# Kernel optimization log

Hardware: AMD Instinct MI355X
Metric: run time of the kernel (lower is better)

Reference implementation:

```python
import jax, jax.numpy as jnp
import numpy as np

B = 512      # batch (len(missing_type))
HALF = 12    # prompt_length // 3
D = 12       # prompt_depth
DT = 512     # text embed dim
DI = 768     # image embed dim
E = DT + DI  # 1280, concat dim
R = 16
H = E // R    # 80
HC = DT // R  # 32
EPS = 1e-5


def _ln(x, g, b):
    m = jnp.mean(x, -1, keepdims=True)
    v = jnp.mean((x - m) ** 2, -1, keepdims=True)
    return (x - m) * jax.lax.rsqrt(v + EPS) * g + b


def _mlp(x, w1, b1, w2, b2):
    return jax.nn.gelu(x @ w1 + b1, approximate=False) @ w2 + b2


def setup_inputs() -> dict:
    key = jax.random.key(0)
    ks = jax.random.split(key, 20)
    n = lambda k, s: jax.random.normal(k, s, dtype=jnp.float32) * 0.02
    return {
        "missing_type": jax.random.randint(ks[0], (B,), 0, 3),
        "vpc": n(ks[1], (HALF, DI)), "vpm": n(ks[2], (HALF, DI)),
        "tpc": n(ks[3], (HALF, DT)), "tpm": n(ks[4], (HALF, DT)),
        "cpc": n(ks[5], (HALF, DT)), "cpi": n(ks[6], (HALF, DT)), "cpt": n(ks[7], (HALF, DT)),
        "ln_img_g": jnp.ones((D, E)), "ln_img_b": jnp.zeros((D, E)),
        "ln_txt_g": jnp.ones((D, E)), "ln_txt_b": jnp.zeros((D, E)),
        "img_w1": n(ks[8], (D, E, H)), "img_b1": jnp.zeros((D, H)),
        "img_w2": n(ks[9], (D, H, DI)), "img_b2": jnp.zeros((D, DI)),
        "txt_w1": n(ks[10], (D, E, H)), "txt_b1": jnp.zeros((D, H)),
        "txt_w2": n(ks[11], (D, H, DT)), "txt_b2": jnp.zeros((D, DT)),
        "cimg_w1": n(ks[12], (DT, HC)), "cimg_b1": jnp.zeros((HC,)),
        "cimg_w2": n(ks[13], (HC, DI)), "cimg_b2": jnp.zeros((DI,)),
        "ctxt_w1": n(ks[14], (DT, HC)), "ctxt_b1": jnp.zeros((HC,)),
        "ctxt_w2": n(ks[15], (HC, DT)), "ctxt_b2": jnp.zeros((DT,)),
    }


def reference(missing_type, vpc, vpm, tpc, tpm, cpc, cpi, cpt,
              ln_img_g, ln_img_b, ln_txt_g, ln_txt_b,
              img_w1, img_b1, img_w2, img_b2,
              txt_w1, txt_b1, txt_w2, txt_b2,
              cimg_w1, cimg_b1, cimg_w2, cimg_b2,
              ctxt_w1, ctxt_b1, ctxt_w2, ctxt_b2):
    depth = img_w1.shape[0]
    mt = missing_type
    # per-sample branch selection, vectorized over the batch
    img = jnp.where((mt == 2)[:, None, None], vpm[None], vpc[None])  # [B,HALF,768]
    txt = jnp.where((mt == 1)[:, None, None], tpm[None], tpc[None])  # [B,HALF,512]
    common = jnp.stack([cpc, cpi, cpt])[mt]                          # [B,HALF,512]
    imgs, txts = [], []
    for d in range(depth):  # sequential depth dependency
        x = jnp.concatenate([img, txt], -1)  # [B,HALF,1280]
        img = _mlp(_ln(x, ln_img_g[d], ln_img_b[d]), img_w1[d], img_b1[d], img_w2[d], img_b2[d])
        txt = _mlp(_ln(x, ln_txt_g[d], ln_txt_b[d]), txt_w1[d], txt_b1[d], txt_w2[d], txt_b2[d])
        imgs.append(img)
        txts.append(txt)
    # depth-0 prompts get the projected common prompt appended along tokens
    img0 = jnp.concatenate([imgs[0], _mlp(common, cimg_w1, cimg_b1, cimg_w2, cimg_b2)], axis=1)
    txt0 = jnp.concatenate([txts[0], _mlp(common, ctxt_w1, ctxt_b1, ctxt_w2, ctxt_b2)], axis=1)
    return (img0, txt0, jnp.stack(imgs[1:]), jnp.stack(txts[1:]))
```

## Files before the change

kernel.cpp:

```cpp
#include <hip/hip_runtime.h>

typedef unsigned int u32;
typedef unsigned short u16;

#define TPB 640
#define NSLOT_TOT 180
#define SLOT_F32 10240
#define CHAIN_DYN 92928

namespace {
constexpr size_t F_BLOB = 0;
constexpr size_t F_S1   = 1843200;
constexpr size_t F_T1   = 1845120;
constexpr size_t F_XI   = 1847040;
constexpr size_t F_XT   = 2178816;
constexpr size_t F_CI   = 2400000;
constexpr size_t F_CT   = 2427648;
constexpr size_t F_END  = 2446080;
constexpr size_t F_XI_U = 0, F_XT_U = 331776, F_CI_U = 552960, F_CT_U = 580608;
}

__device__ __forceinline__ float bflo(u32 u) { return __uint_as_float(u << 16); }
__device__ __forceinline__ float bfhi(u32 u) { return __uint_as_float(u & 0xffff0000u); }
__device__ __forceinline__ float gelu_f(float x) { return 0.5f * x * (1.0f + erff(x * 0.70710678118654752f)); }
__device__ __forceinline__ u16 f2bf(float f) {
    u32 u = __float_as_uint(f);
    u += 0x7fffu + ((u >> 16) & 1u);
    return (u16)(u >> 16);
}

struct P {
    const float *vpc, *vpm, *tpc, *tpm, *cpc, *cpi, *cpt;
    const float *lig, *lib, *ltg, *ltb;
    const float *iw1, *ib1, *iw2, *ib2;
    const float *tw1, *tb1, *tw2, *tb2;
    const float *ciw1, *cib1, *ciw2, *cib2;
    const float *ctw1, *ctb1, *ctw2, *ctb2;
    const u16 *blob;
    const float *s1, *t1;
    float *xi, *xt, *cimg, *ctxt;
};

__global__ __launch_bounds__(256) void prep_pack_kernel(P p, u32* blob32) {
    constexpr u32 N1 = 12u * 1280 * 80;
    constexpr u32 N2 = 12u * 80 * 640;
    u32 i = blockIdx.x * 256 + threadIdx.x;
    if (i < N1) {
        u32 j2 = i % 80, rem = i / 80;
        u32 k = rem % 1280, d = rem / 1280;
        u32 j0 = 2 * j2;
        const int path = (j0 >= 80);
        const float* W = (path ? p.tw1 : p.iw1) + ((size_t)(d * 1280) + k) * 80 + (j0 - 80 * path);
        float g = (path ? p.ltg : p.lig)[d * 1280 + k];
        float2 v = *reinterpret_cast<const float2*>(W);
        blob32[(size_t)d * 153600 + (size_t)k * 80 + j2] =
            (u32)f2bf(g * v.x) | ((u32)f2bf(g * v.y) << 16);
    } else {
        u32 ii = i - N1;
        if (ii >= N2) return;
        u32 c2 = ii % 640, rem = ii / 640;
        u32 k = rem % 80, d = rem / 80;
        u32 c0 = 2 * c2;
        const float* s = (c0 < 768) ? (p.iw2 + ((size_t)(d * 80) + k) * 768 + c0)
                                    : (p.tw2 + ((size_t)(d * 80) + k) * 512 + (c0 - 768));
        float2 v = *reinterpret_cast<const float2*>(s);
        blob32[(size_t)d * 153600 + 102400 + (size_t)k * 640 + c2] =
            (u32)f2bf(v.x) | ((u32)f2bf(v.y) << 16);
    }
}

__global__ __launch_bounds__(TPB) void prep_fold_kernel(P p, float* s1o, float* t1o) {
    __shared__ float sA[8][80], sB[8][80];
    const int tid = threadIdx.x;
    const int d = blockIdx.x >> 1, path = blockIdx.x & 1;
    const float* W1 = (path ? p.tw1 : p.iw1) + (size_t)d * 1280 * 80;
    const float* G  = (path ? p.ltg : p.lig) + d * 1280;
    const float* Bb = (path ? p.ltb : p.lib) + d * 1280;
    const int j = tid % 80, kc = tid / 80;
    float S = 0.f, T = 0.f;
    for (int k = kc * 160; k < kc * 160 + 160; ++k) {
        float w = W1[(size_t)k * 80 + j];
        S += G[k] * w; T += Bb[k] * w;
    }
    sA[kc][j] = S; sB[kc][j] = T;
    __syncthreads();
    if (tid < 80) {
        float Ss = 0.f, Ts = 0.f;
        #pragma unroll
        for (int q = 0; q < 8; ++q) { Ss += sA[q][tid]; Ts += sB[q][tid]; }
        s1o[d * 160 + path * 80 + tid] = Ss;
        t1o[d * 160 + path * 80 + tid] = Ts + (path ? p.tb1 : p.ib1)[d * 80 + tid];
    }
}

__device__ __forceinline__ void stage_slot(const u16* blob, float* buf, int sigma) {
    const int d = sigma / 15, s = sigma % 15;
    const char* gbase = (const char*)(blob + (size_t)d * 307200
                                      + (s < 10 ? (size_t)s * 20480 : 204800 + (size_t)(s - 10) * 20480));
    char* lbase = (char*)buf;
    const int lane = threadIdx.x & 63, wave = threadIdx.x >> 6;
    #pragma unroll
    for (int r = 0; r < 4; ++r) {
        const int q = r * 10 + wave;
        __builtin_amdgcn_global_load_lds(
            (const __attribute__((address_space(1))) void*)(gbase + q * 1024 + lane * 16),
            (__attribute__((address_space(3))) void*)(lbase + q * 1024), 16, 0, 0);
    }
}

#define SLOT_SYNC do { asm volatile("s_waitcnt vmcnt(0)" ::: "memory"); \
                       __builtin_amdgcn_sched_barrier(0); __syncthreads(); } while (0)

__global__ __launch_bounds__(TPB) void chain4_kernel(P p) {
    extern __shared__ float smem[];
    float* buf0 = smem;
    float* buf1 = smem + 10240;
    float* sx   = smem + 20480;
    float* part = smem + 21760;
    float* hh   = smem + 23040;
    float* redA = smem + 23200;
    float* redB = smem + 23210;
    float* st   = smem + 23220;

    const int tid = threadIdx.x, blk = blockIdx.x;

    if (blk < 36) {
        const int v = blk / 12, t = blk % 12;
        stage_slot(p.blob, buf0, 0);
        const float* is = (v == 2) ? p.vpm : p.vpc;
        const float* ts = (v == 1) ? p.tpm : p.tpc;
        for (int k = tid; k < 768; k += TPB) sx[k] = is[t * 768 + k];
        if (tid < 512) sx[768 + tid] = ts[t * 512 + tid];
        SLOT_SYNC;
        int cur = 0;
        const int jp = tid % 80, kc = tid / 80;

        for (int d = 0; d < 12; ++d) {
            {
                float x0 = sx[tid], x1 = sx[tid + 640];
                float s = x0 + x1, s2 = x0 * x0 + x1 * x1;
                #pragma unroll
                for (int off = 32; off > 0; off >>= 1) { s += __shfl_down(s, off); s2 += __shfl_down(s2, off); }
                if ((tid & 63) == 0) { redA[tid >> 6] = s; redB[tid >> 6] = s2; }
            }
            __syncthreads();
            if (tid == 0) {
                float S = 0.f, S2 = 0.f;
                #pragma unroll
                for (int w = 0; w < 10; ++w) { S += redA[w]; S2 += redB[w]; }
                float m = S * (1.0f / 1280.0f);
                float var = S2 * (1.0f / 1280.0f) - m * m;
                st[0] = m; st[1] = rsqrtf(var + 1e-5f);
            }
            float a0 = 0.f, a1 = 0.f, b0 = 0.f, b1 = 0.f;
            for (int s = 0; s < 10; ++s) {
                const int sig = d * 15 + s;
                if (sig + 1 < NSLOT_TOT) stage_slot(p.blob, cur ? buf0 : buf1, sig + 1);
                const u32* wp = (const u32*)(cur ? buf1 : buf0) + kc * 1280 + jp;
                const float* xs = sx + s * 128 + kc * 16;
                #pragma unroll
                for (int i = 0; i < 16; ++i) {
                    u32 w = wp[i * 80];
                    float xv = xs[i];
                    a0 += xv * bflo(w); a1 += xv * bfhi(w);
                }
                if (s == 9) { part[kc * 160 + 2 * jp] = a0; part[kc * 160 + 2 * jp + 1] = a1; }
                SLOT_SYNC; cur ^= 1;
            }
            if (tid < 160) {
                float y = 0.f;
                #pragma unroll
                for (int q = 0; q < 8; ++q) y += part[q * 160 + tid];
                const float m = st[0], rs = st[1];
                hh[tid] = gelu_f(rs * y - m * rs * p.s1[d * 160 + tid] + p.t1[d * 160 + tid]);
            }
            __syncthreads();
            for (int s = 10; s < 15; ++s) {
                const int sig = d * 15 + s;
                if (sig + 1 < NSLOT_TOT) stage_slot(p.blob, cur ? buf0 : buf1, sig + 1);
                const u32* wq = (const u32*)(cur ? buf1 : buf0) + tid;
                const float* hb = hh + ((tid >= 384) ? 80 : 0) + (s - 10) * 16;
                #pragma unroll
                for (int i = 0; i < 16; ++i) {
                    u32 w = wq[i * 640];
                    float hv = hb[i];
                    b0 += hv * bflo(w); b1 += hv * bfhi(w);
                }
                SLOT_SYNC; cur ^= 1;
            }
            {
                const int c0 = 2 * tid;
                const int pth = (c0 >= 768);
                const int cc = c0 - 768 * pth;
                const int Np = pth ? 512 : 768;
                const float* bb = (pth ? p.tb2 : p.ib2) + d * Np + cc;
                float o0 = b0 + bb[0], o1 = b1 + bb[1];
                sx[c0] = o0; sx[c0 + 1] = o1;
                float* xo = pth ? (p.xt + ((size_t)(d * 36) + blk) * 512 + cc)
                                : (p.xi + ((size_t)(d * 36) + blk) * 768 + cc);
                *reinterpret_cast<float2*>(xo) = make_float2(o0, o1);
            }
            __syncthreads();
        }
    } else {
        float* cx  = smem;
        float* ph  = smem + 512;
        float* hhl = smem + 768;
        const int rr = blk - 36, v = rr / 12, t = rr % 12;
        const float* cs = (v == 0) ? p.cpc : (v == 1) ? p.cpi : p.cpt;
        if (tid < 512) cx[tid] = cs[t * 512 + tid];
        __syncthreads();
        if (tid < 256) {
            const int o = tid & 63, kcq = tid >> 6;
            const int path = o >> 5, j = o & 31;
            const float* w = (path ? p.ctw1 : p.ciw1) + (size_t)(kcq * 128) * 32 + j;
            float a = 0.f;
            #pragma unroll 8
            for (int i = 0; i < 128; ++i) { a += cx[kcq * 128 + i] * (*w); w += 32; }
            ph[kcq * 64 + o] = a;
        }
        __syncthreads();
        if (tid < 64) {
            const int path = tid >> 5, j = tid & 31;
            float a = (path ? p.ctb1 : p.cib1)[j];
            #pragma unroll
            for (int q = 0; q < 4; ++q) a += ph[q * 64 + tid];
            hhl[tid] = gelu_f(a);
        }
        __syncthreads();
        for (int o = tid; o < 1280; o += TPB) {
            if (o < 768) {
                float a = p.cib2[o];
                #pragma unroll
                for (int k = 0; k < 32; ++k) a += hhl[k] * p.ciw2[k * 768 + o];
                p.cimg[rr * 768 + o] = a;
            } else {
                const int oo = o - 768;
                float a = p.ctb2[oo];
                #pragma unroll
                for (int k = 0; k < 32; ++k) a += hhl[32 + k] * p.ctw2[k * 512 + oo];
                p.ctxt[rr * 512 + oo] = a;
            }
        }
    }
}

__global__ __launch_bounds__(TPB) void chain_fb_kernel(P p) {
    __shared__ float smem[6592];
    float* sx   = smem;
    float* xln0 = smem + 1280;
    float* xln1 = smem + 2560;
    float* part = smem + 3840;
    float* hh   = smem + 6400;
    float* redA = smem + 6560;
    float* redB = smem + 6570;
    float* st   = smem + 6580;
    const int tid = threadIdx.x, blk = blockIdx.x;
    if (blk < 36) {
        const int v = blk / 12, t = blk % 12;
        const float* is = (v == 2) ? p.vpm : p.vpc;
        const float* ts = (v == 1) ? p.tpm : p.tpc;
        if (tid < 512) sx[768 + tid] = ts[t * 512 + tid];
        for (int k = tid; k < 768; k += TPB) sx[k] = is[t * 768 + k];
        __syncthreads();
        for (int d = 0; d < 12; ++d) {
            {
                float x0 = sx[tid], x1 = sx[tid + 640];
                float s = x0 + x1, s2 = x0 * x0 + x1 * x1;
                #pragma unroll
                for (int off = 32; off > 0; off >>= 1) { s += __shfl_down(s, off); s2 += __shfl_down(s2, off); }
                if ((tid & 63) == 0) { redA[tid >> 6] = s; redB[tid >> 6] = s2; }
            }
            __syncthreads();
            if (tid == 0) {
                float S = 0.f, S2 = 0.f;
                #pragma unroll
                for (int w = 0; w < 10; ++w) { S += redA[w]; S2 += redB[w]; }
                float m = S * (1.0f / 1280.0f);
                float var = S2 * (1.0f / 1280.0f) - m * m;
                st[0] = m; st[1] = rsqrtf(var + 1e-5f);
            }
            __syncthreads();
            const float m = st[0], rs = st[1];
            #pragma unroll
            for (int q = 0; q < 2; ++q) {
                const int k = tid + 640 * q;
                float xc = (sx[k] - m) * rs;
                xln0[k] = xc * p.lig[d * 1280 + k] + p.lib[d * 1280 + k];
                xln1[k] = xc * p.ltg[d * 1280 + k] + p.ltb[d * 1280 + k];
            }
            __syncthreads();
            {
                const int g = tid % 40, kcq = tid / 40;
                const int j0 = 4 * g;
                const float* xl = (j0 >= 80) ? xln1 : xln0;
                const int k0 = kcq * 80;
                float a0 = 0.f, a1 = 0.f, a2 = 0.f, a3 = 0.f;
                const float* wp = (j0 < 80) ? (p.iw1 + ((size_t)(d * 1280) + k0) * 80 + j0)
                                            : (p.tw1 + ((size_t)(d * 1280) + k0) * 80 + (j0 - 80));
                #pragma unroll 8
                for (int i = 0; i < 80; ++i) {
                    float4 w = *reinterpret_cast<const float4*>(wp);
                    float xv = xl[k0 + i];
                    a0 += xv * w.x; a1 += xv * w.y; a2 += xv * w.z; a3 += xv * w.w;
                    wp += 80;
                }
                *reinterpret_cast<float4*>(part + kcq * 160 + j0) = make_float4(a0, a1, a2, a3);
            }
            __syncthreads();
            if (tid < 160) {
                const int path = tid >= 80, j = tid - 80 * path;
                float a = (path ? p.tb1 : p.ib1)[d * 80 + j];
                #pragma unroll
                for (int q = 0; q < 16; ++q) a += part[q * 160 + tid];
                hh[tid] = gelu_f(a);
            }
            __syncthreads();
            {
                const int c = tid;
                const int pth = (c >= 384);
                const int cc = 2 * c - 768 * pth;
                const float* hb = hh + 80 * pth;
                const int Np = pth ? 512 : 768;
                const float* b2 = (pth ? p.tb2 : p.ib2) + d * Np + cc;
                float a0 = b2[0], a1 = b2[1];
                const float* wp = (pth ? p.tw2 + (size_t)(d * 80) * 512 : p.iw2 + (size_t)(d * 80) * 768) + cc;
                #pragma unroll 16
                for (int k = 0; k < 80; ++k) {
                    float2 w = *reinterpret_cast<const float2*>(wp);
                    float hv = hb[k];
                    a0 += hv * w.x; a1 += hv * w.y;
                    wp += Np;
                }
                sx[2 * c] = a0; sx[2 * c + 1] = a1;
                float* xo = pth ? (p.xt + ((size_t)(d * 36) + blk) * 512 + cc)
                                : (p.xi + ((size_t)(d * 36) + blk) * 768 + cc);
                *reinterpret_cast<float2*>(xo) = make_float2(a0, a1);
            }
            __syncthreads();
        }
    } else {
        float* cx  = smem;
        float* ph  = smem + 512;
        float* hhl = smem + 768;
        const int rr = blk - 36, v = rr / 12, t = rr % 12;
        const float* cs = (v == 0) ? p.cpc : (v == 1) ? p.cpi : p.cpt;
        if (tid < 512) cx[tid] = cs[t * 512 + tid];
        __syncthreads();
        if (tid < 256) {
            const int o = tid & 63, kcq = tid >> 6;
            const int path = o >> 5, j = o & 31;
            const float* w = (path ? p.ctw1 : p.ciw1) + (size_t)(kcq * 128) * 32 + j;
            float a = 0.f;
            #pragma unroll 8
            for (int i = 0; i < 128; ++i) { a += cx[kcq * 128 + i] * (*w); w += 32; }
            ph[kcq * 64 + o] = a;
        }
        __syncthreads();
        if (tid < 64) {
            const int path = tid >> 5, j = tid & 31;
            float a = (path ? p.ctb1 : p.cib1)[j];
            #pragma unroll
            for (int q = 0; q < 4; ++q) a += ph[q * 64 + tid];
            hhl[tid] = gelu_f(a);
        }
        __syncthreads();
        for (int o = tid; o < 1280; o += TPB) {
            if (o < 768) {
                float a = p.cib2[o];
                #pragma unroll
                for (int k = 0; k < 32; ++k) a += hhl[k] * p.ciw2[k * 768 + o];
                p.cimg[rr * 768 + o] = a;
            } else {
                const int oo = o - 768;
                float a = p.ctb2[oo];
                #pragma unroll
                for (int k = 0; k < 32; ++k) a += hhl[32 + k] * p.ctw2[k * 512 + oo];
                p.ctxt[rr * 512 + oo] = a;
            }
        }
    }
}

__global__ __launch_bounds__(256) void emit_kernel(const int* __restrict__ mt,
                                                   const float* __restrict__ xi,
                                                   const float* __restrict__ xt,
                                                   const float* __restrict__ cimg,
                                                   const float* __restrict__ ctxt,
                                                   float* __restrict__ out) {
    constexpr unsigned int C0 = 512u * 24 * 192;
    constexpr unsigned int C1 = 512u * 24 * 128;
    constexpr unsigned int C2 = 11u * 512 * 12 * 192;
    constexpr unsigned int C3 = 11u * 512 * 12 * 128;
    constexpr unsigned int TOT = C0 + C1 + C2 + C3;
    const unsigned int stride = gridDim.x * blockDim.x;
    for (unsigned int c = blockIdx.x * blockDim.x + threadIdx.x; c < TOT; c += stride) {
        const float* src;
        if (c < C0) {
            unsigned int b = c / 4608u, r = c % 4608u;
            unsigned int tok = r / 192u, col = (r % 192u) * 4u;
            int v = mt[b];
            src = (tok < 12u) ? xi + ((size_t)v * 12 + tok) * 768 + col
                              : cimg + ((size_t)v * 12 + (tok - 12u)) * 768 + col;
        } else if (c < C0 + C1) {
            unsigned int cc = c - C0;
            unsigned int b = cc / 3072u, r = cc % 3072u;
            unsigned int tok = r / 128u, col = (r % 128u) * 4u;
            int v = mt[b];
            src = (tok < 12u) ? xt + ((size_t)v * 12 + tok) * 512 + col
                              : ctxt + ((size_t)v * 12 + (tok - 12u)) * 512 + col;
        } else if (c < C0 + C1 + C2) {
            unsigned int cc = c - C0 - C1;
            unsigned int d = cc / 1179648u, r = cc % 1179648u;
            unsigned int b = r / 2304u, rr = r % 2304u;
            unsigned int tok = rr / 192u, col = (rr % 192u) * 4u;
            int v = mt[b];
            src = xi + ((size_t)(d + 1) * 36 + v * 12 + tok) * 768 + col;
        } else {
            unsigned int cc = c - C0 - C1 - C2;
            unsigned int d = cc / 786432u, r = cc % 786432u;
            unsigned int b = r / 1536u, rr = r % 1536u;
            unsigned int tok = rr / 128u, col = (rr % 128u) * 4u;
            int v = mt[b];
            src = xt + ((size_t)(d + 1) * 36 + v * 12 + tok) * 512 + col;
        }
        *reinterpret_cast<float4*>(out + (size_t)c * 4) = *reinterpret_cast<const float4*>(src);
    }
}

extern "C" void kernel_launch(void* const* d_in, const int* in_sizes, int n_in,
                              void* d_out, int out_size, void* d_ws, size_t ws_size,
                              hipStream_t stream) {
    const int* mt = (const int*)d_in[0];
    float* ws = (float*)d_ws;
    P p;
    p.vpc  = (const float*)d_in[1];
    p.vpm  = (const float*)d_in[2];
    p.tpc  = (const float*)d_in[3];
    p.tpm  = (const float*)d_in[4];
    p.cpc  = (const float*)d_in[5];
    p.cpi  = (const float*)d_in[6];
    p.cpt  = (const float*)d_in[7];
    p.lig  = (const float*)d_in[8];
    p.lib  = (const float*)d_in[9];
    p.ltg  = (const float*)d_in[10];
    p.ltb  = (const float*)d_in[11];
    p.iw1  = (const float*)d_in[12];
    p.ib1  = (const float*)d_in[13];
    p.iw2  = (const float*)d_in[14];
    p.ib2  = (const float*)d_in[15];
    p.tw1  = (const float*)d_in[16];
    p.tb1  = (const float*)d_in[17];
    p.tw2  = (const float*)d_in[18];
    p.tb2  = (const float*)d_in[19];
    p.ciw1 = (const float*)d_in[20];
    p.cib1 = (const float*)d_in[21];
    p.ciw2 = (const float*)d_in[22];
    p.cib2 = (const float*)d_in[23];
    p.ctw1 = (const float*)d_in[24];
    p.ctb1 = (const float*)d_in[25];
    p.ctw2 = (const float*)d_in[26];
    p.ctb2 = (const float*)d_in[27];

    const bool packed = (ws_size >= F_END * sizeof(float));
    if (packed) {
        p.blob = (const u16*)(ws + F_BLOB);
        p.s1   = ws + F_S1;
        p.t1   = ws + F_T1;
        p.xi   = ws + F_XI;
        p.xt   = ws + F_XT;
        p.cimg = ws + F_CI;
        p.ctxt = ws + F_CT;
        constexpr u32 NPAIR = 12u * 1280 * 80 + 12u * 80 * 640;
        prep_pack_kernel<<<dim3((NPAIR + 255) / 256), dim3(256), 0, stream>>>(p, (u32*)(ws + F_BLOB));
        prep_fold_kernel<<<dim3(24), dim3(TPB), 0, stream>>>(p, ws + F_S1, ws + F_T1);
        hipFuncSetAttribute((const void*)chain4_kernel,
                            hipFuncAttributeMaxDynamicSharedMemorySize, CHAIN_DYN);
        chain4_kernel<<<dim3(72), dim3(TPB), CHAIN_DYN, stream>>>(p);
    } else {
        p.blob = nullptr; p.s1 = nullptr; p.t1 = nullptr;
        p.xi   = ws + F_XI_U;
        p.xt   = ws + F_XT_U;
        p.cimg = ws + F_CI_U;
        p.ctxt = ws + F_CT_U;
        chain_fb_kernel<<<dim3(72), dim3(TPB), 0, stream>>>(p);
    }
    emit_kernel<<<dim3(4096), dim3(256), 0, stream>>>(mt, p.xi, p.xt, p.cimg, p.ctxt, (float*)d_out);
}
```

Before: 252.4 us.

## Switch weight staging to a triple-buffered ring with partial vmcnt waits

Replaces the double-buffered weight slot staging with a three-slot LDS ring that prefetches two slots ahead. Each slot now waits only with vmcnt(4), which lets the next slot's loads stay in flight across the barrier instead of draining all global loads. The per-depth hidden reduction and GELU step is folded into the first second-layer slot, so its separate full barrier goes away. In exchange the kernel uses more LDS per block and relies on fragile manual waitcnt and barrier ordering to stay correct.

```diff
diff --git a/kernel.cpp b/kernel.cpp
--- a/kernel.cpp
+++ b/kernel.cpp
@@ -6,7 +6,7 @@
 #define TPB 640
 #define NSLOT_TOT 180
 #define SLOT_F32 10240
-#define CHAIN_DYN 92928
+#define CHAIN_DYN 133888
 
 namespace {
 constexpr size_t F_BLOB = 0;
@@ -108,31 +108,37 @@
     }
 }
 
-#define SLOT_SYNC do { asm volatile("s_waitcnt vmcnt(0)" ::: "memory"); \
-                       __builtin_amdgcn_sched_barrier(0); __syncthreads(); } while (0)
-
-__global__ __launch_bounds__(TPB) void chain4_kernel(P p) {
+#define CWAIT4 do { asm volatile("s_waitcnt vmcnt(4) lgkmcnt(0)" ::: "memory"); \
+                    __builtin_amdgcn_sched_barrier(0); __builtin_amdgcn_s_barrier(); \
+                    __builtin_amdgcn_sched_barrier(0); } while (0)
+#define CWAIT0 do { asm volatile("s_waitcnt vmcnt(0) lgkmcnt(0)" ::: "memory"); \
+                    __builtin_amdgcn_sched_barrier(0); __builtin_amdgcn_s_barrier(); \
+                    __builtin_amdgcn_sched_barrier(0); } while (0)
+#define LBAR   do { asm volatile("s_waitcnt lgkmcnt(0)" ::: "memory"); \
+                    __builtin_amdgcn_sched_barrier(0); __builtin_amdgcn_s_barrier(); \
+                    __builtin_amdgcn_sched_barrier(0); } while (0)
+
+__global__ __launch_bounds__(TPB) void chain5_kernel(P p) {
     extern __shared__ float smem[];
-    float* buf0 = smem;
-    float* buf1 = smem + 10240;
-    float* sx   = smem + 20480;
-    float* part = smem + 21760;
-    float* hh   = smem + 23040;
-    float* redA = smem + 23200;
-    float* redB = smem + 23210;
-    float* st   = smem + 23220;
+    float* ring = smem;
+    float* sx   = smem + 30720;
+    float* part = smem + 32000;
+    float* hh   = smem + 33280;
+    float* redA = smem + 33440;
+    float* redB = smem + 33450;
+    float* st   = smem + 33460;
 
     const int tid = threadIdx.x, blk = blockIdx.x;
 
     if (blk < 36) {
         const int v = blk / 12, t = blk % 12;
-        stage_slot(p.blob, buf0, 0);
+        stage_slot(p.blob, ring, 0);
+        stage_slot(p.blob, ring + SLOT_F32, 1);
         const float* is = (v == 2) ? p.vpm : p.vpc;
         const float* ts = (v == 1) ? p.tpm : p.tpc;
         for (int k = tid; k < 768; k += TPB) sx[k] = is[t * 768 + k];
         if (tid < 512) sx[768 + tid] = ts[t * 512 + tid];
-        SLOT_SYNC;
-        int cur = 0;
+        CWAIT0;
         const int jp = tid % 80, kc = tid / 80;
 
         for (int d = 0; d < 12; ++d) {
@@ -143,7 +149,7 @@
                 for (int off = 32; off > 0; off >>= 1) { s += __shfl_down(s, off); s2 += __shfl_down(s2, off); }
                 if ((tid & 63) == 0) { redA[tid >> 6] = s; redB[tid >> 6] = s2; }
             }
-            __syncthreads();
+            LBAR;
             if (tid == 0) {
                 float S = 0.f, S2 = 0.f;
                 #pragma unroll
@@ -155,8 +161,9 @@
             float a0 = 0.f, a1 = 0.f, b0 = 0.f, b1 = 0.f;
             for (int s = 0; s < 10; ++s) {
                 const int sig = d * 15 + s;
-                if (sig + 1 < NSLOT_TOT) stage_slot(p.blob, cur ? buf0 : buf1, sig + 1);
-                const u32* wp = (const u32*)(cur ? buf1 : buf0) + kc * 1280 + jp;
+                if (sig == NSLOT_TOT - 1) { CWAIT0; } else { CWAIT4; }
+                if (sig + 2 < NSLOT_TOT) stage_slot(p.blob, ring + (size_t)((sig + 2) % 3) * SLOT_F32, sig + 2);
+                const u32* wp = (const u32*)(ring + (size_t)(sig % 3) * SLOT_F32) + kc * 1280 + jp;
                 const float* xs = sx + s * 128 + kc * 16;
                 #pragma unroll
                 for (int i = 0; i < 16; ++i) {
@@ -165,20 +172,22 @@
                     a0 += xv * bflo(w); a1 += xv * bfhi(w);
                 }
                 if (s == 9) { part[kc * 160 + 2 * jp] = a0; part[kc * 160 + 2 * jp + 1] = a1; }
-                SLOT_SYNC; cur ^= 1;
-            }
-            if (tid < 160) {
-                float y = 0.f;
-                #pragma unroll
-                for (int q = 0; q < 8; ++q) y += part[q * 160 + tid];
-                const float m = st[0], rs = st[1];
-                hh[tid] = gelu_f(rs * y - m * rs * p.s1[d * 160 + tid] + p.t1[d * 160 + tid]);
-            }
-            __syncthreads();
+            }
             for (int s = 10; s < 15; ++s) {
                 const int sig = d * 15 + s;
-                if (sig + 1 < NSLOT_TOT) stage_slot(p.blob, cur ? buf0 : buf1, sig + 1);
-                const u32* wq = (const u32*)(cur ? buf1 : buf0) + tid;
+                if (sig == NSLOT_TOT - 1) { CWAIT0; } else { CWAIT4; }
+                if (sig + 2 < NSLOT_TOT) stage_slot(p.blob, ring + (size_t)((sig + 2) % 3) * SLOT_F32, sig + 2);
+                if (s == 10) {
+                    if (tid < 160) {
+                        float y = 0.f;
+                        #pragma unroll
+                        for (int q = 0; q < 8; ++q) y += part[q * 160 + tid];
+                        const float m = st[0], rs = st[1];
+                        hh[tid] = gelu_f(rs * y - m * rs * p.s1[d * 160 + tid] + p.t1[d * 160 + tid]);
+                    }
+                    LBAR;
+                }
+                const u32* wq = (const u32*)(ring + (size_t)(sig % 3) * SLOT_F32) + tid;
                 const float* hb = hh + ((tid >= 384) ? 80 : 0) + (s - 10) * 16;
                 #pragma unroll
                 for (int i = 0; i < 16; ++i) {
@@ -186,7 +195,6 @@
                     float hv = hb[i];
                     b0 += hv * bflo(w); b1 += hv * bfhi(w);
                 }
-                SLOT_SYNC; cur ^= 1;
             }
             {
                 const int c0 = 2 * tid;
@@ -200,7 +208,7 @@
                                 : (p.xi + ((size_t)(d * 36) + blk) * 768 + cc);
                 *reinterpret_cast<float2*>(xo) = make_float2(o0, o1);
             }
-            __syncthreads();
+            LBAR;
         }
     } else {
         float* cx  = smem;
@@ -474,9 +482,9 @@
         constexpr u32 NPAIR = 12u * 1280 * 80 + 12u * 80 * 640;
         prep_pack_kernel<<<dim3((NPAIR + 255) / 256), dim3(256), 0, stream>>>(p, (u32*)(ws + F_BLOB));
         prep_fold_kernel<<<dim3(24), dim3(TPB), 0, stream>>>(p, ws + F_S1, ws + F_T1);
-        hipFuncSetAttribute((const void*)chain4_kernel,
+        hipFuncSetAttribute((const void*)chain5_kernel,
                             hipFuncAttributeMaxDynamicSharedMemorySize, CHAIN_DYN);
-        chain4_kernel<<<dim3(72), dim3(TPB), CHAIN_DYN, stream>>>(p);
+        chain5_kernel<<<dim3(72), dim3(TPB), CHAIN_DYN, stream>>>(p);
     } else {
         p.blob = nullptr; p.s1 = nullptr; p.t1 = nullptr;
         p.xi   = ws + F_XI_U;
```

Result: slower. 491.0 us (+94.5%).

## Read packed weights directly from global memory instead of double-buffered LDS staging

Applied to the files above, without the earlier changes.

The chain kernel no longer streams each weight slot into LDS through async global_load_lds with a barrier per slot. Each thread now reads the bf16-packed weights straight from global/L2, using 8-byte loads for the first matmul with a 16-way k split, and one pass over 80 rows for the second. This removes 15 block-wide syncs per depth and frees most of the shared memory. It gives up the explicit prefetch overlap and relies on cache for latency hiding. Separately, the emit kernel now copies 8 floats per thread instead of 4.

```diff
diff --git a/kernel.cpp b/kernel.cpp
--- a/kernel.cpp
+++ b/kernel.cpp
@@ -4,9 +4,6 @@
 typedef unsigned short u16;
 
 #define TPB 640
-#define NSLOT_TOT 180
-#define SLOT_F32 10240
-#define CHAIN_DYN 92928
 
 namespace {
 constexpr size_t F_BLOB = 0;
@@ -93,47 +90,28 @@
     }
 }
 
-__device__ __forceinline__ void stage_slot(const u16* blob, float* buf, int sigma) {
-    const int d = sigma / 15, s = sigma % 15;
-    const char* gbase = (const char*)(blob + (size_t)d * 307200
-                                      + (s < 10 ? (size_t)s * 20480 : 204800 + (size_t)(s - 10) * 20480));
-    char* lbase = (char*)buf;
-    const int lane = threadIdx.x & 63, wave = threadIdx.x >> 6;
-    #pragma unroll
-    for (int r = 0; r < 4; ++r) {
-        const int q = r * 10 + wave;
-        __builtin_amdgcn_global_load_lds(
-            (const __attribute__((address_space(1))) void*)(gbase + q * 1024 + lane * 16),
-            (__attribute__((address_space(3))) void*)(lbase + q * 1024), 16, 0, 0);
-    }
-}
-
-#define SLOT_SYNC do { asm volatile("s_waitcnt vmcnt(0)" ::: "memory"); \
-                       __builtin_amdgcn_sched_barrier(0); __syncthreads(); } while (0)
-
-__global__ __launch_bounds__(TPB) void chain4_kernel(P p) {
-    extern __shared__ float smem[];
-    float* buf0 = smem;
-    float* buf1 = smem + 10240;
-    float* sx   = smem + 20480;
-    float* part = smem + 21760;
-    float* hh   = smem + 23040;
-    float* redA = smem + 23200;
-    float* redB = smem + 23210;
-    float* st   = smem + 23220;
+__global__ __launch_bounds__(TPB) void chain6_kernel(P p) {
+    __shared__ float smem[4032];
+    float* sx   = smem;
+    float* part = smem + 1280;
+    float* hh   = smem + 3840;
+    float* redA = smem + 4000;
+    float* redB = smem + 4010;
+    float* st   = smem + 4020;
 
     const int tid = threadIdx.x, blk = blockIdx.x;
 
     if (blk < 36) {
         const int v = blk / 12, t = blk % 12;
-        stage_slot(p.blob, buf0, 0);
         const float* is = (v == 2) ? p.vpm : p.vpc;
         const float* ts = (v == 1) ? p.tpm : p.tpc;
         for (int k = tid; k < 768; k += TPB) sx[k] = is[t * 768 + k];
         if (tid < 512) sx[768 + tid] = ts[t * 512 + tid];
-        SLOT_SYNC;
-        int cur = 0;
-        const int jp = tid % 80, kc = tid / 80;
+        __syncthreads();
+
+        const u32* blob32 = (const u32*)p.blob;
+        const int g = tid % 40, kc = tid / 40;
+        const int j0 = 4 * g;
 
         for (int d = 0; d < 12; ++d) {
             {
@@ -152,53 +130,48 @@
                 float var = S2 * (1.0f / 1280.0f) - m * m;
                 st[0] = m; st[1] = rsqrtf(var + 1e-5f);
             }
-            float a0 = 0.f, a1 = 0.f, b0 = 0.f, b1 = 0.f;
-            for (int s = 0; s < 10; ++s) {
-                const int sig = d * 15 + s;
-                if (sig + 1 < NSLOT_TOT) stage_slot(p.blob, cur ? buf0 : buf1, sig + 1);
-                const u32* wp = (const u32*)(cur ? buf1 : buf0) + kc * 1280 + jp;
-                const float* xs = sx + s * 128 + kc * 16;
-                #pragma unroll
-                for (int i = 0; i < 16; ++i) {
-                    u32 w = wp[i * 80];
-                    float xv = xs[i];
-                    a0 += xv * bflo(w); a1 += xv * bfhi(w);
+            {
+                const int k0 = kc * 80;
+                const u32* wp = blob32 + (size_t)d * 153600 + (size_t)k0 * 80 + 2 * g;
+                float a0 = 0.f, a1 = 0.f, a2 = 0.f, a3 = 0.f;
+                #pragma unroll 16
+                for (int i = 0; i < 80; ++i) {
+                    uint2 w = *reinterpret_cast<const uint2*>(wp);
+                    float xv = sx[k0 + i];
+                    a0 += xv * bflo(w.x); a1 += xv * bfhi(w.x);
+                    a2 += xv * bflo(w.y); a3 += xv * bfhi(w.y);
+                    wp += 80;
                 }
-                if (s == 9) { part[kc * 160 + 2 * jp] = a0; part[kc * 160 + 2 * jp + 1] = a1; }
-                SLOT_SYNC; cur ^= 1;
-            }
+                *reinterpret_cast<float4*>(part + kc * 160 + j0) = make_float4(a0, a1, a2, a3);
+            }
+            __syncthreads();
             if (tid < 160) {
                 float y = 0.f;
                 #pragma unroll
-                for (int q = 0; q < 8; ++q) y += part[q * 160 + tid];
+                for (int q = 0; q < 16; ++q) y += part[q * 160 + tid];
                 const float m = st[0], rs = st[1];
                 hh[tid] = gelu_f(rs * y - m * rs * p.s1[d * 160 + tid] + p.t1[d * 160 + tid]);
             }
             __syncthreads();
-            for (int s = 10; s < 15; ++s) {
-                const int sig = d * 15 + s;
-                if (sig + 1 < NSLOT_TOT) stage_slot(p.blob, cur ? buf0 : buf1, sig + 1);
-                const u32* wq = (const u32*)(cur ? buf1 : buf0) + tid;
-                const float* hb = hh + ((tid >= 384) ? 80 : 0) + (s - 10) * 16;
-                #pragma unroll
-                for (int i = 0; i < 16; ++i) {
-                    u32 w = wq[i * 640];
-                    float hv = hb[i];
-                    b0 += hv * bflo(w); b1 += hv * bfhi(w);
+            {
+                const int c = tid;
+                const int pth = (c >= 384);
+                const int cc = 2 * c - 768 * pth;
+                const float* hb = hh + 80 * pth;
+                const u32* wq = blob32 + (size_t)d * 153600 + 102400 + c;
+                const float* bb = (pth ? p.tb2 : p.ib2) + d * (pth ? 512 : 768) + cc;
+                float a0 = bb[0], a1 = bb[1];
+                #pragma unroll 16
+                for (int k = 0; k < 80; ++k) {
+                    u32 w = *wq;
+                    float hv = hb[k];
+                    a0 += hv * bflo(w); a1 += hv * bfhi(w);
+                    wq += 640;
                 }
-                SLOT_SYNC; cur ^= 1;
-            }
-            {
-                const int c0 = 2 * tid;
-                const int pth = (c0 >= 768);
-                const int cc = c0 - 768 * pth;
-                const int Np = pth ? 512 : 768;
-                const float* bb = (pth ? p.tb2 : p.ib2) + d * Np + cc;
-                float o0 = b0 + bb[0], o1 = b1 + bb[1];
-                sx[c0] = o0; sx[c0 + 1] = o1;
+                sx[2 * c] = a0; sx[2 * c + 1] = a1;
                 float* xo = pth ? (p.xt + ((size_t)(d * 36) + blk) * 512 + cc)
                                 : (p.xi + ((size_t)(d * 36) + blk) * 768 + cc);
-                *reinterpret_cast<float2*>(xo) = make_float2(o0, o1);
+                *reinterpret_cast<float2*>(xo) = make_float2(a0, a1);
             }
             __syncthreads();
         }
@@ -388,43 +361,47 @@
                                                    const float* __restrict__ cimg,
                                                    const float* __restrict__ ctxt,
                                                    float* __restrict__ out) {
-    constexpr unsigned int C0 = 512u * 24 * 192;
-    constexpr unsigned int C1 = 512u * 24 * 128;
-    constexpr unsigned int C2 = 11u * 512 * 12 * 192;
-    constexpr unsigned int C3 = 11u * 512 * 12 * 128;
+    constexpr unsigned int C0 = 512u * 24 * 96;
+    constexpr unsigned int C1 = 512u * 24 * 64;
+    constexpr unsigned int C2 = 11u * 512 * 12 * 96;
+    constexpr unsigned int C3 = 11u * 512 * 12 * 64;
     constexpr unsigned int TOT = C0 + C1 + C2 + C3;
     const unsigned int stride = gridDim.x * blockDim.x;
     for (unsigned int c = blockIdx.x * blockDim.x + threadIdx.x; c < TOT; c += stride) {
         const float* src;
         if (c < C0) {
-            unsigned int b = c / 4608u, r = c % 4608u;
-            unsigned int tok = r / 192u, col = (r % 192u) * 4u;
+            unsigned int b = c / 2304u, r = c % 2304u;
+            unsigned int tok = r / 96u, col = (r % 96u) * 8u;
             int v = mt[b];
             src = (tok < 12u) ? xi + ((size_t)v * 12 + tok) * 768 + col
                               : cimg + ((size_t)v * 12 + (tok - 12u)) * 768 + col;
         } else if (c < C0 + C1) {
             unsigned int cc = c - C0;
-            unsigned int b = cc / 3072u, r = cc % 3072u;
-            unsigned int tok = r / 128u, col = (r % 128u) * 4u;
+            unsigned int b = cc / 1536u, r = cc % 1536u;
+            unsigned int tok = r / 64u, col = (r % 64u) * 8u;
             int v = mt[b];
             src = (tok < 12u) ? xt + ((size_t)v * 12 + tok) * 512 + col
                               : ctxt + ((size_t)v * 12 + (tok - 12u)) * 512 + col;
         } else if (c < C0 + C1 + C2) {
             unsigned int cc = c - C0 - C1;
-            unsigned int d = cc / 1179648u, r = cc % 1179648u;
-            unsigned int b = r / 2304u, rr = r % 2304u;
-            unsigned int tok = rr / 192u, col = (rr % 192u) * 4u;
+            unsigned int d = cc / 589824u, r = cc % 589824u;
+            unsigned int b = r / 1152u, rr = r % 1152u;
+            unsigned int tok = rr / 96u, col = (rr % 96u) * 8u;
             int v = mt[b];
             src = xi + ((size_t)(d + 1) * 36 + v * 12 + tok) * 768 + col;
         } else {
             unsigned int cc = c - C0 - C1 - C2;
-            unsigned int d = cc / 786432u, r = cc % 786432u;
-            unsigned int b = r / 1536u, rr = r % 1536u;
-            unsigned int tok = rr / 128u, col = (rr % 128u) * 4u;
+            unsigned int d = cc / 393216u, r = cc % 393216u;
+            unsigned int b = r / 768u, rr = r % 768u;
+            unsigned int tok = rr / 64u, col = (rr % 64u) * 8u;
             int v = mt[b];
             src = xt + ((size_t)(d + 1) * 36 + v * 12 + tok) * 512 + col;
         }
-        *reinterpret_cast<float4*>(out + (size_t)c * 4) = *reinterpret_cast<const float4*>(src);
+        float4 f0 = *reinterpret_cast<const float4*>(src);
+        float4 f1 = *reinterpret_cast<const float4*>(src + 4);
+        float* dst = out + (size_t)c * 8;
+        *reinterpret_cast<float4*>(dst)     = f0;
+        *reinterpret_cast<float4*>(dst + 4) = f1;
     }
 }
 
@@ -474,9 +451,7 @@
         constexpr u32 NPAIR = 12u * 1280 * 80 + 12u * 80 * 640;
         prep_pack_kernel<<<dim3((NPAIR + 255) / 256), dim3(256), 0, stream>>>(p, (u32*)(ws + F_BLOB));
         prep_fold_kernel<<<dim3(24), dim3(TPB), 0, stream>>>(p, ws + F_S1, ws + F_T1);
-        hipFuncSetAttribute((const void*)chain4_kernel,
-                            hipFuncAttributeMaxDynamicSharedMemorySize, CHAIN_DYN);
-        chain4_kernel<<<dim3(72), dim3(TPB), CHAIN_DYN, stream>>>(p);
+        chain6_kernel<<<dim3(72), dim3(TPB), 0, stream>>>(p);
     } else {
         p.blob = nullptr; p.s1 = nullptr; p.t1 = nullptr;
         p.xi   = ws + F_XI_U;
```

Result: faster. 224.1 us (-11.2%).
